# Performance work log

Measured on AMD Instinct MI355X. Metric: run time of the kernel, lower is better.

The kernel has to match this reference:

```python
import jax, jax.numpy as jnp
import numpy as np

N, S, D, H = 2, 2048, 1024, 16
DH = D // H  # 64


def setup_inputs() -> dict:
    key = jax.random.key(0)
    ks = jax.random.split(key, 7)
    scale = 1.0 / np.sqrt(DH)  # ~nn.Linear default init range
    return {
        "sequences": jax.random.normal(ks[0], (N, S, D), dtype=jnp.float32),
        "Wq": jax.random.uniform(ks[1], (H, DH, DH), jnp.float32, -scale, scale),
        "bq": jax.random.uniform(ks[2], (H, DH), jnp.float32, -scale, scale),
        "Wk": jax.random.uniform(ks[3], (H, DH, DH), jnp.float32, -scale, scale),
        "bk": jax.random.uniform(ks[4], (H, DH), jnp.float32, -scale, scale),
        "Wv": jax.random.uniform(ks[5], (H, DH, DH), jnp.float32, -scale, scale),
        "bv": jax.random.uniform(ks[6], (H, DH), jnp.float32, -scale, scale),
    }


def reference(sequences, Wq, bq, Wk, bk, Wv, bv):
    n, s, d = sequences.shape
    x = sequences.reshape(n, s, H, DH)  # [N,S,H,Dh]
    # per-head Linear: y = x @ W^T + b, batched over heads
    q = jnp.einsum('nshd,hed->nshe', x, Wq) + bq  # [N,S,H,Dh]
    k = jnp.einsum('nshd,hed->nshe', x, Wk) + bk
    v = jnp.einsum('nshd,hed->nshe', x, Wv) + bv
    # attention: scores [N,H,S,S]
    scores = jnp.einsum('nqhd,nkhd->nhqk', q, k) / jnp.sqrt(jnp.float32(DH))
    w = jax.nn.softmax(scores, axis=-1)
    out = jnp.einsum('nhqk,nkhd->nqhd', w, v)  # [N,S,H,Dh]
    return out.reshape(n, s, d)
```

## Files before the change

### kernel.cpp

```cpp
#include <hip/hip_runtime.h>
#include <hip/hip_bf16.h>


#define NB 2
#define SS 2048
#define DM 1024
#define NH 16
#define DHd 64

typedef __attribute__((ext_vector_type(8))) short bf16x8;
typedef __attribute__((ext_vector_type(4))) float f32x4;

union U8 { bf16x8 v; unsigned short u[8]; };

__device__ __forceinline__ unsigned short f2b(float x) {
    __hip_bfloat16 h = __float2bfloat16(x);
    return *reinterpret_cast<unsigned short*>(&h);
}

__device__ __forceinline__ bf16x8 pack8(float4 a, float4 b) {
    U8 t;
    t.u[0] = f2b(a.x); t.u[1] = f2b(a.y); t.u[2] = f2b(a.z); t.u[3] = f2b(a.w);
    t.u[4] = f2b(b.x); t.u[5] = f2b(b.y); t.u[6] = f2b(b.z); t.u[7] = f2b(b.w);
    return t.v;
}

__device__ __forceinline__ int swz(int row, int ch) {
    return row * 64 + ((ch ^ (row & 7)) * 8);
}

#define QSCALE 0.18033688011112042f

__global__ __launch_bounds__(256) void qkv_proj(
    const float* __restrict__ seq,
    const float* __restrict__ Wq, const float* __restrict__ bq,
    const float* __restrict__ Wk, const float* __restrict__ bk,
    const float* __restrict__ Wv, const float* __restrict__ bv,
    unsigned short* __restrict__ Q, unsigned short* __restrict__ K,
    unsigned short* __restrict__ Vt)
{
    __shared__ unsigned short Xl[128 * 64];
    __shared__ unsigned short Wl[3 * 64 * 64];
    __shared__ unsigned short Ol[128 * 72];

    const int tid = threadIdx.x;
    const int wv = tid >> 6, L = tid & 63, lo = L & 15, qd = L >> 4;
    const int bi = blockIdx.x;
    const int nh = bi >> 4, sb = bi & 15;
    const int h = nh & (NH - 1), n = nh >> 4;
    const int s0 = sb * 128;

#pragma unroll
    for (int i = 0; i < 4; ++i) {
        int idx = tid + i * 256;
        int r = idx >> 3, ch = idx & 7;
        const float* src = seq + ((size_t)(n * SS + s0 + r)) * DM + h * DHd + ch * 8;
        float4 a = ((const float4*)src)[0];
        float4 b = ((const float4*)src)[1];
        *(bf16x8*)&Xl[swz(r, ch)] = pack8(a, b);
    }
#pragma unroll
    for (int i = 0; i < 6; ++i) {
        int idx = tid + i * 256;
        int mat = idx >> 9;
        int rem = idx & 511;
        int e = rem >> 3, ch = rem & 7;
        const float* Wm = (mat == 0) ? Wq : (mat == 1) ? Wk : Wv;
        const float* src = Wm + (size_t)(h * DHd + e) * DHd + ch * 8;
        float4 a = ((const float4*)src)[0];
        float4 b = ((const float4*)src)[1];
        *(bf16x8*)&Wl[mat * 4096 + swz(e, ch)] = pack8(a, b);
    }
    __syncthreads();

    bf16x8 xf[2][2];
#pragma unroll
    for (int st = 0; st < 2; ++st)
#pragma unroll
        for (int kt = 0; kt < 2; ++kt)
            xf[st][kt] = *(const bf16x8*)&Xl[swz(wv * 32 + st * 16 + lo, kt * 4 + qd)];

#pragma unroll
    for (int m2 = 0; m2 < 2; ++m2) {
        const unsigned short* Wb = &Wl[m2 * 4096];
        const float* bias = m2 ? bk : bq;
        unsigned short* O = m2 ? K : Q;
        const float sc = m2 ? 1.0f : QSCALE;

        f32x4 acc[4][2];
#pragma unroll
        for (int et = 0; et < 4; ++et) {
            float4 bb = *(const float4*)&bias[h * DHd + et * 16 + qd * 4];
#pragma unroll
            for (int st = 0; st < 2; ++st)
                acc[et][st] = (f32x4){bb.x, bb.y, bb.z, bb.w};
        }
#pragma unroll
        for (int et = 0; et < 4; ++et) {
            bf16x8 wf0 = *(const bf16x8*)&Wb[swz(et * 16 + lo, qd)];
            bf16x8 wf1 = *(const bf16x8*)&Wb[swz(et * 16 + lo, 4 + qd)];
#pragma unroll
            for (int st = 0; st < 2; ++st) {
                acc[et][st] = __builtin_amdgcn_mfma_f32_16x16x32_bf16(
                    wf0, xf[st][0], acc[et][st], 0, 0, 0);
                acc[et][st] = __builtin_amdgcn_mfma_f32_16x16x32_bf16(
                    wf1, xf[st][1], acc[et][st], 0, 0, 0);
            }
        }
        if (m2) __syncthreads();
#pragma unroll
        for (int et = 0; et < 4; ++et)
#pragma unroll
            for (int st = 0; st < 2; ++st) {
                int s = wv * 32 + st * 16 + lo;
                ushort4 w;
                w.x = f2b(acc[et][st][0] * sc); w.y = f2b(acc[et][st][1] * sc);
                w.z = f2b(acc[et][st][2] * sc); w.w = f2b(acc[et][st][3] * sc);
                *(ushort4*)&Ol[s * 72 + et * 16 + qd * 4] = w;
            }
        __syncthreads();
        {
            const int sl = tid >> 3, e0 = (tid & 7) * 8;
#pragma unroll
            for (int i = 0; i < 4; ++i) {
                bf16x8 v = *(const bf16x8*)&Ol[(i * 32 + sl) * 72 + e0];
                *(bf16x8*)&O[((size_t)nh * SS + s0 + i * 32 + sl) * DHd + e0] = v;
            }
        }
    }

    {
        const unsigned short* Wb = &Wl[2 * 4096];
        float bvv[4];
#pragma unroll
        for (int et = 0; et < 4; ++et) bvv[et] = bv[h * DHd + et * 16 + lo];

        f32x4 acc[2][4];
#pragma unroll
        for (int st = 0; st < 2; ++st)
#pragma unroll
            for (int et = 0; et < 4; ++et)
                acc[st][et] = (f32x4){bvv[et], bvv[et], bvv[et], bvv[et]};
#pragma unroll
        for (int et = 0; et < 4; ++et) {
            bf16x8 wf0 = *(const bf16x8*)&Wb[swz(et * 16 + lo, qd)];
            bf16x8 wf1 = *(const bf16x8*)&Wb[swz(et * 16 + lo, 4 + qd)];
#pragma unroll
            for (int st = 0; st < 2; ++st) {
                acc[st][et] = __builtin_amdgcn_mfma_f32_16x16x32_bf16(
                    xf[st][0], wf0, acc[st][et], 0, 0, 0);
                acc[st][et] = __builtin_amdgcn_mfma_f32_16x16x32_bf16(
                    xf[st][1], wf1, acc[st][et], 0, 0, 0);
            }
        }
        __syncthreads();
#pragma unroll
        for (int st = 0; st < 2; ++st)
#pragma unroll
            for (int et = 0; et < 4; ++et) {
                int e = et * 16 + lo;
                int s = wv * 32 + st * 16 + qd * 4;
                ushort4 w;
                w.x = f2b(acc[st][et][0]); w.y = f2b(acc[st][et][1]);
                w.z = f2b(acc[st][et][2]); w.w = f2b(acc[st][et][3]);
                *(ushort4*)&Ol[e * 136 + s] = w;
            }
        __syncthreads();
        {
            const int er = tid >> 4, s8 = (tid & 15) * 8;
#pragma unroll
            for (int i = 0; i < 4; ++i) {
                int e = i * 16 + er;
                bf16x8 v = *(const bf16x8*)&Ol[e * 136 + s8];
                *(bf16x8*)&Vt[((size_t)nh * DHd + e) * SS + s0 + s8] = v;
            }
        }
    }
}

#define PSTR 72
#define THR 3.0f
#define NT (SS / 64)

__global__ __launch_bounds__(256) void attn(
    const unsigned short* __restrict__ Qg, const unsigned short* __restrict__ Kg,
    const unsigned short* __restrict__ Vg, float* __restrict__ out)
{
    __shared__ unsigned short Kl[2][64 * 64];
    __shared__ unsigned short Vl[2][64 * 64];
    __shared__ unsigned short Pl[4][32 * PSTR];

    const int tid = threadIdx.x;
    const int wv = tid >> 6, L = tid & 63, lo = L & 15, qd = L >> 4;
    const int bi = blockIdx.x;
    const int nh = bi >> 4, qblk = bi & 15;
    const int h = nh & (NH - 1), n = nh >> 4;
    const int q0 = qblk * 128 + wv * 32;

    const unsigned short* Qnh = Qg + (size_t)nh * SS * DHd;
    const unsigned short* Knh = Kg + (size_t)nh * SS * DHd;
    const unsigned short* Vnh = Vg + (size_t)nh * DHd * SS;

    const int r0 = tid >> 3, c0 = tid & 7;

    bf16x8 qf[2][2];
#pragma unroll
    for (int ct = 0; ct < 2; ++ct)
#pragma unroll
        for (int kt = 0; kt < 2; ++kt)
            qf[ct][kt] = *(const bf16x8*)(Qnh + (size_t)(q0 + ct * 16 + lo) * DHd
                                          + kt * 32 + qd * 8);

    f32x4 oacc[4][2];
#pragma unroll
    for (int rt = 0; rt < 4; ++rt)
#pragma unroll
        for (int ct = 0; ct < 2; ++ct)
            oacc[rt][ct] = (f32x4){0.f, 0.f, 0.f, 0.f};

    float m[2] = {-1e30f, -1e30f};
    float l[2] = {0.f, 0.f};

    uint4 ks0 = *(const uint4*)(Knh + (size_t)r0 * DHd + c0 * 8);
    uint4 ks1 = *(const uint4*)(Knh + (size_t)(r0 + 32) * DHd + c0 * 8);
    uint4 vs0 = *(const uint4*)(Vnh + (size_t)r0 * SS + c0 * 8);
    uint4 vs1 = *(const uint4*)(Vnh + (size_t)(r0 + 32) * SS + c0 * 8);
    *(uint4*)&Kl[0][swz(r0, c0)]      = ks0;
    *(uint4*)&Kl[0][swz(r0 + 32, c0)] = ks1;
    *(uint4*)&Vl[0][swz(r0, c0)]      = vs0;
    *(uint4*)&Vl[0][swz(r0 + 32, c0)] = vs1;
    ks0 = *(const uint4*)(Knh + (size_t)(64 + r0) * DHd + c0 * 8);
    ks1 = *(const uint4*)(Knh + (size_t)(64 + r0 + 32) * DHd + c0 * 8);
    vs0 = *(const uint4*)(Vnh + (size_t)r0 * SS + 64 + c0 * 8);
    vs1 = *(const uint4*)(Vnh + (size_t)(r0 + 32) * SS + 64 + c0 * 8);
    __syncthreads();

    for (int t = 0; t < NT; ++t) {
        const int cur = t & 1;

        f32x4 sacc[4][2];
#pragma unroll
        for (int rt = 0; rt < 4; ++rt)
#pragma unroll
            for (int ct = 0; ct < 2; ++ct)
                sacc[rt][ct] = (f32x4){0.f, 0.f, 0.f, 0.f};
        __builtin_amdgcn_s_setprio(1);
#pragma unroll
        for (int rt = 0; rt < 4; ++rt)
#pragma unroll
            for (int kt = 0; kt < 2; ++kt) {
                bf16x8 kf = *(const bf16x8*)&Kl[cur][swz(rt * 16 + lo, kt * 4 + qd)];
#pragma unroll
                for (int ct = 0; ct < 2; ++ct)
                    sacc[rt][ct] = __builtin_amdgcn_mfma_f32_16x16x32_bf16(
                        kf, qf[ct][kt], sacc[rt][ct], 0, 0, 0);
            }
        __builtin_amdgcn_s_setprio(0);

#pragma unroll
        for (int ct = 0; ct < 2; ++ct) {
            float mx = sacc[0][ct][0];
#pragma unroll
            for (int rt = 0; rt < 4; ++rt)
#pragma unroll
                for (int r = 0; r < 4; ++r)
                    mx = fmaxf(mx, sacc[rt][ct][r]);
            mx = fmaxf(mx, __shfl_xor(mx, 16, 64));
            mx = fmaxf(mx, __shfl_xor(mx, 32, 64));
            if (__any(mx > m[ct] + THR)) {
                const float mn = fmaxf(m[ct], mx);
                const float corr = __builtin_amdgcn_exp2f(m[ct] - mn);
                l[ct] *= corr;
#pragma unroll
                for (int rt = 0; rt < 4; ++rt)
#pragma unroll
                    for (int r = 0; r < 4; ++r)
                        oacc[rt][ct][r] *= corr;
                m[ct] = mn;
            }
            const float mb = m[ct];
            float rs = 0.f;
#pragma unroll
            for (int rt = 0; rt < 4; ++rt) {
                float p0 = __builtin_amdgcn_exp2f(sacc[rt][ct][0] - mb);
                float p1 = __builtin_amdgcn_exp2f(sacc[rt][ct][1] - mb);
                float p2 = __builtin_amdgcn_exp2f(sacc[rt][ct][2] - mb);
                float p3 = __builtin_amdgcn_exp2f(sacc[rt][ct][3] - mb);
                rs += (p0 + p1) + (p2 + p3);
                ushort4 w;
                w.x = f2b(p0); w.y = f2b(p1); w.z = f2b(p2); w.w = f2b(p3);
                *(ushort4*)&Pl[wv][(ct * 16 + lo) * PSTR + rt * 16 + qd * 4] = w;
            }
            l[ct] += rs;
        }

        __builtin_amdgcn_s_setprio(1);
#pragma unroll
        for (int kt = 0; kt < 2; ++kt) {
            bf16x8 pfr[2];
#pragma unroll
            for (int ct = 0; ct < 2; ++ct)
                pfr[ct] = *(const bf16x8*)&Pl[wv][(ct * 16 + lo) * PSTR
                                                  + kt * 32 + qd * 8];
#pragma unroll
            for (int rt = 0; rt < 4; ++rt) {
                bf16x8 vf = *(const bf16x8*)&Vl[cur][swz(rt * 16 + lo, kt * 4 + qd)];
#pragma unroll
                for (int ct = 0; ct < 2; ++ct)
                    oacc[rt][ct] = __builtin_amdgcn_mfma_f32_16x16x32_bf16(
                        vf, pfr[ct], oacc[rt][ct], 0, 0, 0);
            }
        }
        __builtin_amdgcn_s_setprio(0);

        if (t + 1 < NT) {
            *(uint4*)&Kl[cur ^ 1][swz(r0, c0)]      = ks0;
            *(uint4*)&Kl[cur ^ 1][swz(r0 + 32, c0)] = ks1;
            *(uint4*)&Vl[cur ^ 1][swz(r0, c0)]      = vs0;
            *(uint4*)&Vl[cur ^ 1][swz(r0 + 32, c0)] = vs1;
            if (t + 2 < NT) {
                const int kn = (t + 2) * 64;
                ks0 = *(const uint4*)(Knh + (size_t)(kn + r0) * DHd + c0 * 8);
                ks1 = *(const uint4*)(Knh + (size_t)(kn + r0 + 32) * DHd + c0 * 8);
                vs0 = *(const uint4*)(Vnh + (size_t)r0 * SS + kn + c0 * 8);
                vs1 = *(const uint4*)(Vnh + (size_t)(r0 + 32) * SS + kn + c0 * 8);
            }
        }
        __syncthreads();
    }

#pragma unroll
    for (int ct = 0; ct < 2; ++ct) {
        float lt = l[ct];
        lt += __shfl_xor(lt, 16, 64);
        lt += __shfl_xor(lt, 32, 64);
        const float inv = 1.0f / lt;
        const int s = q0 + ct * 16 + lo;
#pragma unroll
        for (int rt = 0; rt < 4; ++rt) {
            float4 o;
            o.x = oacc[rt][ct][0] * inv; o.y = oacc[rt][ct][1] * inv;
            o.z = oacc[rt][ct][2] * inv; o.w = oacc[rt][ct][3] * inv;
            *(float4*)&out[((size_t)n * SS + s) * DM + h * DHd
                           + rt * 16 + qd * 4] = o;
        }
    }
}

extern "C" void kernel_launch(void* const* d_in, const int* in_sizes, int n_in,
                              void* d_out, int out_size, void* d_ws, size_t ws_size,
                              hipStream_t stream) {
    const float* seq = (const float*)d_in[0];
    const float* Wq  = (const float*)d_in[1];
    const float* bq  = (const float*)d_in[2];
    const float* Wk  = (const float*)d_in[3];
    const float* bk  = (const float*)d_in[4];
    const float* Wv  = (const float*)d_in[5];
    const float* bv  = (const float*)d_in[6];
    float* out = (float*)d_out;

    const size_t per = (size_t)NB * NH * SS * DHd;
    unsigned short* Q  = (unsigned short*)d_ws;
    unsigned short* K  = Q + per;
    unsigned short* Vt = K + per;

    qkv_proj<<<512, 256, 0, stream>>>(seq, Wq, bq, Wk, bk, Wv, bv, Q, K, Vt);
    attn<<<512, 256, 0, stream>>>(Q, K, Vt, out);
}
```

Measured before the change: 140.4 us.

## Load K/V fragments directly from global into registers, dropping LDS staging

```diff
diff --git a/kernel.cpp b/kernel.cpp
--- a/kernel.cpp
+++ b/kernel.cpp
@@ -182,12 +182,10 @@
 #define THR 3.0f
 #define NT (SS / 64)
 
-__global__ __launch_bounds__(256) void attn(
+__global__ __launch_bounds__(256, 2) void attn(
     const unsigned short* __restrict__ Qg, const unsigned short* __restrict__ Kg,
     const unsigned short* __restrict__ Vg, float* __restrict__ out)
 {
-    __shared__ unsigned short Kl[2][64 * 64];
-    __shared__ unsigned short Vl[2][64 * 64];
     __shared__ unsigned short Pl[4][32 * PSTR];
 
     const int tid = threadIdx.x;
@@ -201,8 +199,6 @@
     const unsigned short* Knh = Kg + (size_t)nh * SS * DHd;
     const unsigned short* Vnh = Vg + (size_t)nh * DHd * SS;
 
-    const int r0 = tid >> 3, c0 = tid & 7;
-
     bf16x8 qf[2][2];
 #pragma unroll
     for (int ct = 0; ct < 2; ++ct)
@@ -211,6 +207,18 @@
             qf[ct][kt] = *(const bf16x8*)(Qnh + (size_t)(q0 + ct * 16 + lo) * DHd
                                           + kt * 32 + qd * 8);
 
+    const unsigned short* Kb = Knh + (size_t)lo * DHd + qd * 8;
+    const unsigned short* Vb = Vnh + (size_t)lo * SS + qd * 8;
+
+    bf16x8 kreg[4][2], vreg[4][2];
+#pragma unroll
+    for (int rt = 0; rt < 4; ++rt)
+#pragma unroll
+        for (int kt = 0; kt < 2; ++kt) {
+            kreg[rt][kt] = *(const bf16x8*)(Kb + rt * (16 * DHd) + kt * 32);
+            vreg[rt][kt] = *(const bf16x8*)(Vb + (size_t)rt * (16 * SS) + kt * 32);
+        }
+
     f32x4 oacc[4][2];
 #pragma unroll
     for (int rt = 0; rt < 4; ++rt)
@@ -221,23 +229,7 @@
     float m[2] = {-1e30f, -1e30f};
     float l[2] = {0.f, 0.f};
 
-    uint4 ks0 = *(const uint4*)(Knh + (size_t)r0 * DHd + c0 * 8);
-    uint4 ks1 = *(const uint4*)(Knh + (size_t)(r0 + 32) * DHd + c0 * 8);
-    uint4 vs0 = *(const uint4*)(Vnh + (size_t)r0 * SS + c0 * 8);
-    uint4 vs1 = *(const uint4*)(Vnh + (size_t)(r0 + 32) * SS + c0 * 8);
-    *(uint4*)&Kl[0][swz(r0, c0)]      = ks0;
-    *(uint4*)&Kl[0][swz(r0 + 32, c0)] = ks1;
-    *(uint4*)&Vl[0][swz(r0, c0)]      = vs0;
-    *(uint4*)&Vl[0][swz(r0 + 32, c0)] = vs1;
-    ks0 = *(const uint4*)(Knh + (size_t)(64 + r0) * DHd + c0 * 8);
-    ks1 = *(const uint4*)(Knh + (size_t)(64 + r0 + 32) * DHd + c0 * 8);
-    vs0 = *(const uint4*)(Vnh + (size_t)r0 * SS + 64 + c0 * 8);
-    vs1 = *(const uint4*)(Vnh + (size_t)(r0 + 32) * SS + 64 + c0 * 8);
-    __syncthreads();
-
     for (int t = 0; t < NT; ++t) {
-        const int cur = t & 1;
-
         f32x4 sacc[4][2];
 #pragma unroll
         for (int rt = 0; rt < 4; ++rt)
@@ -248,14 +240,21 @@
 #pragma unroll
         for (int rt = 0; rt < 4; ++rt)
 #pragma unroll
-            for (int kt = 0; kt < 2; ++kt) {
-                bf16x8 kf = *(const bf16x8*)&Kl[cur][swz(rt * 16 + lo, kt * 4 + qd)];
+            for (int kt = 0; kt < 2; ++kt)
 #pragma unroll
                 for (int ct = 0; ct < 2; ++ct)
                     sacc[rt][ct] = __builtin_amdgcn_mfma_f32_16x16x32_bf16(
-                        kf, qf[ct][kt], sacc[rt][ct], 0, 0, 0);
-            }
+                        kreg[rt][kt], qf[ct][kt], sacc[rt][ct], 0, 0, 0);
         __builtin_amdgcn_s_setprio(0);
+
+        if (t + 1 < NT) {
+            const unsigned short* Kn = Kb + (size_t)(t + 1) * 64 * DHd;
+#pragma unroll
+            for (int rt = 0; rt < 4; ++rt)
+#pragma unroll
+                for (int kt = 0; kt < 2; ++kt)
+                    kreg[rt][kt] = *(const bf16x8*)(Kn + rt * (16 * DHd) + kt * 32);
+        }
 
 #pragma unroll
         for (int ct = 0; ct < 2; ++ct) {
@@ -303,30 +302,22 @@
                 pfr[ct] = *(const bf16x8*)&Pl[wv][(ct * 16 + lo) * PSTR
                                                   + kt * 32 + qd * 8];
 #pragma unroll
-            for (int rt = 0; rt < 4; ++rt) {
-                bf16x8 vf = *(const bf16x8*)&Vl[cur][swz(rt * 16 + lo, kt * 4 + qd)];
+            for (int rt = 0; rt < 4; ++rt)
 #pragma unroll
                 for (int ct = 0; ct < 2; ++ct)
                     oacc[rt][ct] = __builtin_amdgcn_mfma_f32_16x16x32_bf16(
-                        vf, pfr[ct], oacc[rt][ct], 0, 0, 0);
-            }
+                        vreg[rt][kt], pfr[ct], oacc[rt][ct], 0, 0, 0);
         }
         __builtin_amdgcn_s_setprio(0);
 
         if (t + 1 < NT) {
-            *(uint4*)&Kl[cur ^ 1][swz(r0, c0)]      = ks0;
-            *(uint4*)&Kl[cur ^ 1][swz(r0 + 32, c0)] = ks1;
-            *(uint4*)&Vl[cur ^ 1][swz(r0, c0)]      = vs0;
-            *(uint4*)&Vl[cur ^ 1][swz(r0 + 32, c0)] = vs1;
-            if (t + 2 < NT) {
-                const int kn = (t + 2) * 64;
-                ks0 = *(const uint4*)(Knh + (size_t)(kn + r0) * DHd + c0 * 8);
-                ks1 = *(const uint4*)(Knh + (size_t)(kn + r0 + 32) * DHd + c0 * 8);
-                vs0 = *(const uint4*)(Vnh + (size_t)r0 * SS + kn + c0 * 8);
-                vs1 = *(const uint4*)(Vnh + (size_t)(r0 + 32) * SS + kn + c0 * 8);
-            }
-        }
-        __syncthreads();
+            const unsigned short* Vn = Vb + (size_t)(t + 1) * 64;
+#pragma unroll
+            for (int rt = 0; rt < 4; ++rt)
+#pragma unroll
+                for (int kt = 0; kt < 2; ++kt)
+                    vreg[rt][kt] = *(const bf16x8*)(Vn + (size_t)rt * (16 * SS) + kt * 32);
+        }
     }
 
 #pragma unroll
```

Result: slower. 200.6 us (+42.9%).

## Halve per-wave query rows in attention and double grid size

Applied to the files above, without the earlier changes.

```diff
diff --git a/kernel.cpp b/kernel.cpp
--- a/kernel.cpp
+++ b/kernel.cpp
@@ -182,20 +182,20 @@
 #define THR 3.0f
 #define NT (SS / 64)
 
-__global__ __launch_bounds__(256) void attn(
+__global__ __launch_bounds__(256, 3) void attn(
     const unsigned short* __restrict__ Qg, const unsigned short* __restrict__ Kg,
     const unsigned short* __restrict__ Vg, float* __restrict__ out)
 {
     __shared__ unsigned short Kl[2][64 * 64];
     __shared__ unsigned short Vl[2][64 * 64];
-    __shared__ unsigned short Pl[4][32 * PSTR];
+    __shared__ unsigned short Pl[4][16 * PSTR];
 
     const int tid = threadIdx.x;
     const int wv = tid >> 6, L = tid & 63, lo = L & 15, qd = L >> 4;
     const int bi = blockIdx.x;
-    const int nh = bi >> 4, qblk = bi & 15;
+    const int nh = bi >> 5, qblk = bi & 31;
     const int h = nh & (NH - 1), n = nh >> 4;
-    const int q0 = qblk * 128 + wv * 32;
+    const int q0 = qblk * 64 + wv * 16;
 
     const unsigned short* Qnh = Qg + (size_t)nh * SS * DHd;
     const unsigned short* Knh = Kg + (size_t)nh * SS * DHd;
@@ -203,23 +203,18 @@
 
     const int r0 = tid >> 3, c0 = tid & 7;
 
-    bf16x8 qf[2][2];
-#pragma unroll
-    for (int ct = 0; ct < 2; ++ct)
-#pragma unroll
-        for (int kt = 0; kt < 2; ++kt)
-            qf[ct][kt] = *(const bf16x8*)(Qnh + (size_t)(q0 + ct * 16 + lo) * DHd
-                                          + kt * 32 + qd * 8);
-
-    f32x4 oacc[4][2];
+    bf16x8 qf[2];
+#pragma unroll
+    for (int kt = 0; kt < 2; ++kt)
+        qf[kt] = *(const bf16x8*)(Qnh + (size_t)(q0 + lo) * DHd + kt * 32 + qd * 8);
+
+    f32x4 oacc[4];
 #pragma unroll
     for (int rt = 0; rt < 4; ++rt)
-#pragma unroll
-        for (int ct = 0; ct < 2; ++ct)
-            oacc[rt][ct] = (f32x4){0.f, 0.f, 0.f, 0.f};
-
-    float m[2] = {-1e30f, -1e30f};
-    float l[2] = {0.f, 0.f};
+        oacc[rt] = (f32x4){0.f, 0.f, 0.f, 0.f};
+
+    float m = -1e30f;
+    float l = 0.f;
 
     uint4 ks0 = *(const uint4*)(Knh + (size_t)r0 * DHd + c0 * 8);
     uint4 ks1 = *(const uint4*)(Knh + (size_t)(r0 + 32) * DHd + c0 * 8);
@@ -238,77 +233,66 @@
     for (int t = 0; t < NT; ++t) {
         const int cur = t & 1;
 
-        f32x4 sacc[4][2];
+        f32x4 sacc[4];
 #pragma unroll
         for (int rt = 0; rt < 4; ++rt)
-#pragma unroll
-            for (int ct = 0; ct < 2; ++ct)
-                sacc[rt][ct] = (f32x4){0.f, 0.f, 0.f, 0.f};
+            sacc[rt] = (f32x4){0.f, 0.f, 0.f, 0.f};
         __builtin_amdgcn_s_setprio(1);
 #pragma unroll
         for (int rt = 0; rt < 4; ++rt)
 #pragma unroll
             for (int kt = 0; kt < 2; ++kt) {
                 bf16x8 kf = *(const bf16x8*)&Kl[cur][swz(rt * 16 + lo, kt * 4 + qd)];
-#pragma unroll
-                for (int ct = 0; ct < 2; ++ct)
-                    sacc[rt][ct] = __builtin_amdgcn_mfma_f32_16x16x32_bf16(
-                        kf, qf[ct][kt], sacc[rt][ct], 0, 0, 0);
+                sacc[rt] = __builtin_amdgcn_mfma_f32_16x16x32_bf16(
+                    kf, qf[kt], sacc[rt], 0, 0, 0);
             }
         __builtin_amdgcn_s_setprio(0);
 
-#pragma unroll
-        for (int ct = 0; ct < 2; ++ct) {
-            float mx = sacc[0][ct][0];
+        {
+            float mx = sacc[0][0];
 #pragma unroll
             for (int rt = 0; rt < 4; ++rt)
 #pragma unroll
                 for (int r = 0; r < 4; ++r)
-                    mx = fmaxf(mx, sacc[rt][ct][r]);
+                    mx = fmaxf(mx, sacc[rt][r]);
             mx = fmaxf(mx, __shfl_xor(mx, 16, 64));
             mx = fmaxf(mx, __shfl_xor(mx, 32, 64));
-            if (__any(mx > m[ct] + THR)) {
-                const float mn = fmaxf(m[ct], mx);
-                const float corr = __builtin_amdgcn_exp2f(m[ct] - mn);
-                l[ct] *= corr;
+            if (__any(mx > m + THR)) {
+                const float mn = fmaxf(m, mx);
+                const float corr = __builtin_amdgcn_exp2f(m - mn);
+                l *= corr;
 #pragma unroll
                 for (int rt = 0; rt < 4; ++rt)
 #pragma unroll
                     for (int r = 0; r < 4; ++r)
-                        oacc[rt][ct][r] *= corr;
-                m[ct] = mn;
-            }
-            const float mb = m[ct];
+                        oacc[rt][r] *= corr;
+                m = mn;
+            }
+            const float mb = m;
             float rs = 0.f;
 #pragma unroll
             for (int rt = 0; rt < 4; ++rt) {
-                float p0 = __builtin_amdgcn_exp2f(sacc[rt][ct][0] - mb);
-                float p1 = __builtin_amdgcn_exp2f(sacc[rt][ct][1] - mb);
-                float p2 = __builtin_amdgcn_exp2f(sacc[rt][ct][2] - mb);
-                float p3 = __builtin_amdgcn_exp2f(sacc[rt][ct][3] - mb);
+                float p0 = __builtin_amdgcn_exp2f(sacc[rt][0] - mb);
+                float p1 = __builtin_amdgcn_exp2f(sacc[rt][1] - mb);
+                float p2 = __builtin_amdgcn_exp2f(sacc[rt][2] - mb);
+                float p3 = __builtin_amdgcn_exp2f(sacc[rt][3] - mb);
                 rs += (p0 + p1) + (p2 + p3);
                 ushort4 w;
                 w.x = f2b(p0); w.y = f2b(p1); w.z = f2b(p2); w.w = f2b(p3);
-                *(ushort4*)&Pl[wv][(ct * 16 + lo) * PSTR + rt * 16 + qd * 4] = w;
-            }
-            l[ct] += rs;
+                *(ushort4*)&Pl[wv][lo * PSTR + rt * 16 + qd * 4] = w;
+            }
+            l += rs;
         }
 
         __builtin_amdgcn_s_setprio(1);
 #pragma unroll
         for (int kt = 0; kt < 2; ++kt) {
-            bf16x8 pfr[2];
-#pragma unroll
-            for (int ct = 0; ct < 2; ++ct)
-                pfr[ct] = *(const bf16x8*)&Pl[wv][(ct * 16 + lo) * PSTR
-                                                  + kt * 32 + qd * 8];
+            bf16x8 pfr = *(const bf16x8*)&Pl[wv][lo * PSTR + kt * 32 + qd * 8];
 #pragma unroll
             for (int rt = 0; rt < 4; ++rt) {
                 bf16x8 vf = *(const bf16x8*)&Vl[cur][swz(rt * 16 + lo, kt * 4 + qd)];
-#pragma unroll
-                for (int ct = 0; ct < 2; ++ct)
-                    oacc[rt][ct] = __builtin_amdgcn_mfma_f32_16x16x32_bf16(
-                        vf, pfr[ct], oacc[rt][ct], 0, 0, 0);
+                oacc[rt] = __builtin_amdgcn_mfma_f32_16x16x32_bf16(
+                    vf, pfr, oacc[rt], 0, 0, 0);
             }
         }
         __builtin_amdgcn_s_setprio(0);
@@ -329,18 +313,17 @@
         __syncthreads();
     }
 
-#pragma unroll
-    for (int ct = 0; ct < 2; ++ct) {
-        float lt = l[ct];
+    {
+        float lt = l;
         lt += __shfl_xor(lt, 16, 64);
         lt += __shfl_xor(lt, 32, 64);
         const float inv = 1.0f / lt;
-        const int s = q0 + ct * 16 + lo;
+        const int s = q0 + lo;
 #pragma unroll
         for (int rt = 0; rt < 4; ++rt) {
             float4 o;
-            o.x = oacc[rt][ct][0] * inv; o.y = oacc[rt][ct][1] * inv;
-            o.z = oacc[rt][ct][2] * inv; o.w = oacc[rt][ct][3] * inv;
+            o.x = oacc[rt][0] * inv; o.y = oacc[rt][1] * inv;
+            o.z = oacc[rt][2] * inv; o.w = oacc[rt][3] * inv;
             *(float4*)&out[((size_t)n * SS + s) * DM + h * DHd
                            + rt * 16 + qd * 4] = o;
         }
@@ -365,5 +348,5 @@
     unsigned short* Vt = K + per;
 
     qkv_proj<<<512, 256, 0, stream>>>(seq, Wq, bq, Wk, bk, Wv, bv, Q, K, Vt);
-    attn<<<512, 256, 0, stream>>>(Q, K, Vt, out);
-}
+    attn<<<1024, 256, 0, stream>>>(Q, K, Vt, out);
+}
```

Measured after the change: 146.7 us. 4.5% more time.

## Stage K/V via direct global-to-LDS loads, remap blocks per XCD, relayout P buffer

Applied to the files above, without the earlier changes.

```diff
diff --git a/kernel.cpp b/kernel.cpp
--- a/kernel.cpp
+++ b/kernel.cpp
@@ -178,7 +178,6 @@
     }
 }
 
-#define PSTR 72
 #define THR 3.0f
 #define NT (SS / 64)
 
@@ -188,12 +187,15 @@
 {
     __shared__ unsigned short Kl[2][64 * 64];
     __shared__ unsigned short Vl[2][64 * 64];
-    __shared__ unsigned short Pl[4][32 * PSTR];
+    __shared__ unsigned short Pl[4][2048];
 
     const int tid = threadIdx.x;
     const int wv = tid >> 6, L = tid & 63, lo = L & 15, qd = L >> 4;
-    const int bi = blockIdx.x;
-    const int nh = bi >> 4, qblk = bi & 15;
+
+    const int orig = blockIdx.x;
+    const int xcd = orig & 7, slot = orig >> 3;
+    const int nh = xcd * 4 + (slot >> 4);
+    const int qblk = slot & 15;
     const int h = nh & (NH - 1), n = nh >> 4;
     const int q0 = qblk * 128 + wv * 32;
 
@@ -201,8 +203,6 @@
     const unsigned short* Knh = Kg + (size_t)nh * SS * DHd;
     const unsigned short* Vnh = Vg + (size_t)nh * DHd * SS;
 
-    const int r0 = tid >> 3, c0 = tid & 7;
-
     bf16x8 qf[2][2];
 #pragma unroll
     for (int ct = 0; ct < 2; ++ct)
@@ -221,22 +221,32 @@
     float m[2] = {-1e30f, -1e30f};
     float l[2] = {0.f, 0.f};
 
-    uint4 ks0 = *(const uint4*)(Knh + (size_t)r0 * DHd + c0 * 8);
-    uint4 ks1 = *(const uint4*)(Knh + (size_t)(r0 + 32) * DHd + c0 * 8);
-    uint4 vs0 = *(const uint4*)(Vnh + (size_t)r0 * SS + c0 * 8);
-    uint4 vs1 = *(const uint4*)(Vnh + (size_t)(r0 + 32) * SS + c0 * 8);
-    *(uint4*)&Kl[0][swz(r0, c0)]      = ks0;
-    *(uint4*)&Kl[0][swz(r0 + 32, c0)] = ks1;
-    *(uint4*)&Vl[0][swz(r0, c0)]      = vs0;
-    *(uint4*)&Vl[0][swz(r0 + 32, c0)] = vs1;
-    ks0 = *(const uint4*)(Knh + (size_t)(64 + r0) * DHd + c0 * 8);
-    ks1 = *(const uint4*)(Knh + (size_t)(64 + r0 + 32) * DHd + c0 * 8);
-    vs0 = *(const uint4*)(Vnh + (size_t)r0 * SS + 64 + c0 * 8);
-    vs1 = *(const uint4*)(Vnh + (size_t)(r0 + 32) * SS + 64 + c0 * 8);
+    auto stage = [&](int b, int kv) {
+#pragma unroll
+        for (int j = 0; j < 2; ++j) {
+            const int r = wv * 16 + j * 8 + (L >> 3);
+            const int cg = (L & 7) ^ (r & 7);
+            const unsigned short* gk = Knh + (size_t)(kv + r) * DHd + cg * 8;
+            const unsigned short* gv = Vnh + (size_t)r * SS + kv + cg * 8;
+            __builtin_amdgcn_global_load_lds(
+                (const __attribute__((address_space(1))) unsigned int*)gk,
+                (__attribute__((address_space(3))) unsigned int*)
+                    &Kl[b][wv * 1024 + j * 512],
+                16, 0, 0);
+            __builtin_amdgcn_global_load_lds(
+                (const __attribute__((address_space(1))) unsigned int*)gv,
+                (__attribute__((address_space(3))) unsigned int*)
+                    &Vl[b][wv * 1024 + j * 512],
+                16, 0, 0);
+        }
+    };
+
+    stage(0, 0);
     __syncthreads();
 
     for (int t = 0; t < NT; ++t) {
         const int cur = t & 1;
+        if (t + 1 < NT) stage(cur ^ 1, (t + 1) * 64);
 
         f32x4 sacc[4][2];
 #pragma unroll
@@ -289,7 +299,8 @@
                 rs += (p0 + p1) + (p2 + p3);
                 ushort4 w;
                 w.x = f2b(p0); w.y = f2b(p1); w.z = f2b(p2); w.w = f2b(p3);
-                *(ushort4*)&Pl[wv][(ct * 16 + lo) * PSTR + rt * 16 + qd * 4] = w;
+                *(ushort4*)&Pl[wv][(2 * rt + (qd >> 1)) * 256
+                                   + (ct * 16 + lo) * 8 + (qd & 1) * 4] = w;
             }
             l[ct] += rs;
         }
@@ -300,8 +311,8 @@
             bf16x8 pfr[2];
 #pragma unroll
             for (int ct = 0; ct < 2; ++ct)
-                pfr[ct] = *(const bf16x8*)&Pl[wv][(ct * 16 + lo) * PSTR
-                                                  + kt * 32 + qd * 8];
+                pfr[ct] = *(const bf16x8*)&Pl[wv][(4 * kt + qd) * 256
+                                                  + (ct * 16 + lo) * 8];
 #pragma unroll
             for (int rt = 0; rt < 4; ++rt) {
                 bf16x8 vf = *(const bf16x8*)&Vl[cur][swz(rt * 16 + lo, kt * 4 + qd)];
@@ -313,19 +324,6 @@
         }
         __builtin_amdgcn_s_setprio(0);
 
-        if (t + 1 < NT) {
-            *(uint4*)&Kl[cur ^ 1][swz(r0, c0)]      = ks0;
-            *(uint4*)&Kl[cur ^ 1][swz(r0 + 32, c0)] = ks1;
-            *(uint4*)&Vl[cur ^ 1][swz(r0, c0)]      = vs0;
-            *(uint4*)&Vl[cur ^ 1][swz(r0 + 32, c0)] = vs1;
-            if (t + 2 < NT) {
-                const int kn = (t + 2) * 64;
-                ks0 = *(const uint4*)(Knh + (size_t)(kn + r0) * DHd + c0 * 8);
-                ks1 = *(const uint4*)(Knh + (size_t)(kn + r0 + 32) * DHd + c0 * 8);
-                vs0 = *(const uint4*)(Vnh + (size_t)r0 * SS + kn + c0 * 8);
-                vs1 = *(const uint4*)(Vnh + (size_t)(r0 + 32) * SS + kn + c0 * 8);
-            }
-        }
         __syncthreads();
     }
 
```

Measured after the change: 145.6 us. 1.04x slower.
